# Kernel tuning notes

Measured on AMD Instinct MI355X. Metric: run time of the kernel, lower is better.

The kernel has to match this reference:

```python
import jax, jax.numpy as jnp
import numpy as np

N = 100000          # nodes
E = 1600000         # edges (before self-loops)
F_IN = 128          # raw node features
TOPO = 8            # topological feature dim
HEADS1, HID1 = 8, 8 # conv1: 8 heads x 8 channels, concat -> 64
C_OUT = 40          # classes (conv2: 1 head, no concat)
NEG_SLOPE = 0.2     # PyG GATConv leaky_relu slope


def setup_inputs() -> dict:
    key = jax.random.key(0)
    ks = jax.random.split(key, 12)
    x = jax.random.normal(ks[0], (N, F_IN), jnp.float32)
    topo = jax.random.normal(ks[1], (N, TOPO), jnp.float32)
    edge_index = jax.random.randint(ks[2], (2, E), 0, N, jnp.int32)
    s = 0.1
    W1 = jax.random.normal(ks[3], (F_IN + TOPO, HEADS1 * HID1), jnp.float32) * s
    a_src1 = jax.random.normal(ks[4], (HEADS1, HID1), jnp.float32) * s
    a_dst1 = jax.random.normal(ks[5], (HEADS1, HID1), jnp.float32) * s
    b1 = jnp.zeros((HEADS1 * HID1,), jnp.float32)
    W2 = jax.random.normal(ks[6], (HEADS1 * HID1, C_OUT), jnp.float32) * s
    a_src2 = jax.random.normal(ks[7], (1, C_OUT), jnp.float32) * s
    a_dst2 = jax.random.normal(ks[8], (1, C_OUT), jnp.float32) * s
    b2 = jnp.zeros((C_OUT,), jnp.float32)
    return {"x": x, "topo": topo, "edge_index": edge_index,
            "W1": W1, "a_src1": a_src1, "a_dst1": a_dst1, "b1": b1,
            "W2": W2, "a_src2": a_src2, "a_dst2": a_dst2, "b2": b2}


def _gat_conv(x, src, dst, W, a_src, a_dst, b, heads, concat):
    # x: [N, Fin]; src/dst: [Etot] (self-loops already included)
    n = x.shape[0]
    h = (x @ W).reshape(n, heads, -1)                 # [N, H, C]
    alpha_s = jnp.sum(h * a_src[None], axis=-1)       # [N, H]
    alpha_d = jnp.sum(h * a_dst[None], axis=-1)       # [N, H]
    e = jax.nn.leaky_relu(alpha_s[src] + alpha_d[dst], NEG_SLOPE)  # [Etot, H]
    # segment softmax over destination nodes (numerically stable)
    m = jax.ops.segment_max(e, dst, num_segments=n)   # [N, H]
    ex = jnp.exp(e - m[dst])
    z = jax.ops.segment_sum(ex, dst, num_segments=n)  # [N, H]
    alpha = ex / (z[dst] + 1e-16)                     # [Etot, H]
    out = jax.ops.segment_sum(h[src] * alpha[..., None], dst, num_segments=n)  # [N,H,C]
    out = out.reshape(n, -1) if concat else out.mean(axis=1)
    return out + b


def reference(x, topo, edge_index, W1, a_src1, a_dst1, b1, W2, a_src2, a_dst2, b2):
    n = x.shape[0]
    loops = jnp.arange(n, dtype=edge_index.dtype)
    src = jnp.concatenate([edge_index[0], loops])  # PyG add_self_loops=True
    dst = jnp.concatenate([edge_index[1], loops])
    h = jnp.concatenate([x, topo], axis=1)         # [N, F_IN + TOPO]
    # dropout is identity in eval mode
    h = jax.nn.elu(_gat_conv(h, src, dst, W1, a_src1, a_dst1, b1, HEADS1, True))
    logits = _gat_conv(h, src, dst, W2, a_src2, a_dst2, b2, 1, False)
    return jax.nn.log_softmax(logits, axis=1)
```

## Files before the change

### kernel.cpp

```cpp
#include <hip/hip_runtime.h>
#include <math.h>


#define NBUK_MAX 512
#define BIN_CHUNK 4096
#define BUK_CAP 4608

typedef unsigned short ushort_t;

__device__ inline unsigned int f2bf(float f) {
    unsigned int u = __float_as_uint(f);
    u += 0x7FFFu + ((u >> 16) & 1u);
    return u >> 16;
}
__device__ inline float bf_lo(unsigned int u) {
    return __uint_as_float(u << 16);
}
__device__ inline float bf_hi(unsigned int u) {
    return __uint_as_float(u & 0xFFFF0000u);
}
__device__ inline float lrelu_exp(float q) {
    return __expf(q >= 0.f ? q : 0.2f * q);
}

__device__ inline int wave_incl_scan(int v, int lane) {
    #pragma unroll
    for (int ofs = 1; ofs < 64; ofs <<= 1) {
        int t = __shfl_up(v, ofs);
        if (lane >= ofs) v += t;
    }
    return v;
}

__global__ __launch_bounds__(256) void k_bin(const int* __restrict__ src,
                                             const int* __restrict__ dst,
                                             int* __restrict__ gCursor,
                                             unsigned int* __restrict__ tmp,
                                             int E, int NBUK) {
    __shared__ int lcnt[NBUK_MAX];
    __shared__ int lcur[NBUK_MAX];
    int tid = threadIdx.x;
    int base = blockIdx.x * BIN_CHUNK;
    for (int i = tid; i < NBUK; i += 256) lcnt[i] = 0;
    __syncthreads();
    int d[16];
    #pragma unroll
    for (int q = 0; q < 4; q++) {
        int e = base + q * 1024 + 4 * tid;
        if (e + 3 < E) {
            int4 v = *(const int4*)&dst[e];
            d[4 * q + 0] = v.x; d[4 * q + 1] = v.y;
            d[4 * q + 2] = v.z; d[4 * q + 3] = v.w;
        } else {
            #pragma unroll
            for (int k = 0; k < 4; k++)
                d[4 * q + k] = (e + k < E) ? dst[e + k] : -1;
        }
    }
    #pragma unroll
    for (int k = 0; k < 16; k++)
        if (d[k] >= 0) atomicAdd(&lcnt[d[k] >> 8], 1);
    __syncthreads();
    for (int b = tid; b < NBUK; b += 256) {
        int c = lcnt[b];
        lcur[b] = c ? b * BUK_CAP + atomicAdd(&gCursor[b], c) : 0;
    }
    __syncthreads();
    #pragma unroll
    for (int q = 0; q < 4; q++) {
        int e = base + q * 1024 + 4 * tid;
        int s[4];
        if (e + 3 < E) {
            int4 v = *(const int4*)&src[e];
            s[0] = v.x; s[1] = v.y; s[2] = v.z; s[3] = v.w;
        } else {
            #pragma unroll
            for (int k = 0; k < 4; k++)
                s[k] = (e + k < E) ? src[e + k] : 0;
        }
        #pragma unroll
        for (int k = 0; k < 4; k++) {
            int dd = d[4 * q + k];
            if (dd >= 0) {
                int p = atomicAdd(&lcur[dd >> 8], 1);
                tmp[p] = ((unsigned int)s[k] << 8) | (unsigned int)(dd & 255);
            }
        }
    }
}

__global__ __launch_bounds__(512) void k_fill2(const unsigned int* __restrict__ tmp,
                                               const int* __restrict__ gCursor,
                                               int* __restrict__ rowptr,
                                               int* __restrict__ rowEnd,
                                               int* __restrict__ csr, int N) {
    __shared__ int cnt[256];
    __shared__ int cur[256];
    __shared__ int wsum[4];
    int b = blockIdx.x, tid = threadIdx.x;
    int e0 = b * BUK_CAP;
    int cnt_e = gCursor[b];
    int e1 = e0 + cnt_e;
    if (tid < 256) cnt[tid] = 0;
    __syncthreads();
    {
        int nq = cnt_e >> 2;
        const uint4* t4 = (const uint4*)(tmp + e0);
        for (int q = tid; q < nq; q += 512) {
            uint4 v = t4[q];
            atomicAdd(&cnt[v.x & 255u], 1);
            atomicAdd(&cnt[v.y & 255u], 1);
            atomicAdd(&cnt[v.z & 255u], 1);
            atomicAdd(&cnt[v.w & 255u], 1);
        }
        for (int i = (nq << 2) + tid; i < cnt_e; i += 512)
            atomicAdd(&cnt[tmp[e0 + i] & 255u], 1);
    }
    __syncthreads();
    if (tid < 256) {
        int lane = tid & 63, wv = tid >> 6;
        int v = cnt[tid];
        int incl = wave_incl_scan(v, lane);
        if (lane == 63) wsum[wv] = incl;
        cnt[tid] = incl - v;
    }
    __syncthreads();
    if (tid < 256) {
        int wv = tid >> 6;
        int woff = 0;
        for (int i = 0; i < wv; i++) woff += wsum[i];
        int excl = woff + cnt[tid];
        int node = b * 256 + tid;
        int start = e0 + excl;
        cur[tid] = start;
        if (node < N) {
            rowptr[node] = start;
        }
    }
    __syncthreads();
    if (tid < 256) {
        int node = b * 256 + tid;
        if (node < N) rowEnd[node] = (tid < 255) ? cur[tid + 1] : e1;
    }
    __syncthreads();
    for (int i = e0 + tid; i < e1; i += 512) {
        unsigned int t = tmp[i];
        int p = atomicAdd(&cur[t & 255u], 1);
        csr[p] = (int)(t >> 8);
    }
}

__global__ __launch_bounds__(256) void k_xform1(const float* __restrict__ x,
                                                const float* __restrict__ topo,
                                                const float* __restrict__ W1,
                                                const float* __restrict__ asrc,
                                                const float* __restrict__ adst,
                                                ushort_t* __restrict__ h1b,
                                                float* __restrict__ as1,
                                                float* __restrict__ ad1, int N) {
    __shared__ float XT[136 * 64];
    __shared__ float WS[136 * 64];
    int tid = threadIdx.x;
    int n0 = blockIdx.x * 64;
    {
        const float4* W4 = (const float4*)W1;
        float4* WS4 = (float4*)WS;
        for (int i = tid; i < 2176; i += 256) WS4[i] = W4[i];
    }
    {
        const float4* x4 = (const float4*)x;
        for (int i = tid; i < 2048; i += 256) {
            int node = i & 63, k4 = i >> 6;
            int gn = n0 + node; if (gn > N - 1) gn = N - 1;
            float4 v = x4[(size_t)gn * 32 + k4];
            int k = k4 * 4;
            XT[(k + 0) * 64 + node] = v.x;
            XT[(k + 1) * 64 + node] = v.y;
            XT[(k + 2) * 64 + node] = v.z;
            XT[(k + 3) * 64 + node] = v.w;
        }
        const float4* t4 = (const float4*)topo;
        if (tid < 128) {
            int node = tid & 63, j4 = tid >> 6;
            int gn = n0 + node; if (gn > N - 1) gn = N - 1;
            float4 v = t4[(size_t)gn * 2 + j4];
            int k = 128 + j4 * 4;
            XT[(k + 0) * 64 + node] = v.x;
            XT[(k + 1) * 64 + node] = v.y;
            XT[(k + 2) * 64 + node] = v.z;
            XT[(k + 3) * 64 + node] = v.w;
        }
    }
    __syncthreads();
    int ci = tid & 15, ni = tid >> 4;
    int nb = ni * 4, cb = ci * 4;
    float acc[16];
    #pragma unroll
    for (int i = 0; i < 16; i++) acc[i] = 0.f;
    #pragma unroll 4
    for (int k = 0; k < 136; k++) {
        float4 xv = *(const float4*)&XT[k * 64 + nb];
        float4 wv = *(const float4*)&WS[k * 64 + cb];
        acc[0]  = fmaf(xv.x, wv.x, acc[0]);  acc[1]  = fmaf(xv.x, wv.y, acc[1]);
        acc[2]  = fmaf(xv.x, wv.z, acc[2]);  acc[3]  = fmaf(xv.x, wv.w, acc[3]);
        acc[4]  = fmaf(xv.y, wv.x, acc[4]);  acc[5]  = fmaf(xv.y, wv.y, acc[5]);
        acc[6]  = fmaf(xv.y, wv.z, acc[6]);  acc[7]  = fmaf(xv.y, wv.w, acc[7]);
        acc[8]  = fmaf(xv.z, wv.x, acc[8]);  acc[9]  = fmaf(xv.z, wv.y, acc[9]);
        acc[10] = fmaf(xv.z, wv.z, acc[10]); acc[11] = fmaf(xv.z, wv.w, acc[11]);
        acc[12] = fmaf(xv.w, wv.x, acc[12]); acc[13] = fmaf(xv.w, wv.y, acc[13]);
        acc[14] = fmaf(xv.w, wv.z, acc[14]); acc[15] = fmaf(xv.w, wv.w, acc[15]);
    }
    int head = cb >> 3;
    #pragma unroll
    for (int i = 0; i < 4; i++) {
        int n = n0 + nb + i;
        unsigned int p0 = f2bf(acc[i * 4 + 0]) | (f2bf(acc[i * 4 + 1]) << 16);
        unsigned int p1 = f2bf(acc[i * 4 + 2]) | (f2bf(acc[i * 4 + 3]) << 16);
        if (n < N) *(uint2*)&h1b[(size_t)n * 64 + cb] = make_uint2(p0, p1);
        float s = 0.f, d = 0.f;
        #pragma unroll
        for (int j = 0; j < 4; j++) {
            s = fmaf(acc[i * 4 + j], asrc[cb + j], s);
            d = fmaf(acc[i * 4 + j], adst[cb + j], d);
        }
        s += __shfl_xor(s, 1);
        d += __shfl_xor(d, 1);
        if ((ci & 1) == 0 && n < N) {
            as1[n * 8 + head] = s;
            ad1[n * 8 + head] = d;
        }
    }
}

__global__ __launch_bounds__(256) void k_agg1(const ushort_t* __restrict__ h1b,
                                              const float* __restrict__ as1,
                                              const float* __restrict__ ad1,
                                              const float* __restrict__ b1,
                                              const int* __restrict__ rowptr,
                                              const int* __restrict__ rowEnd,
                                              const int* __restrict__ csr,
                                              float* __restrict__ h2, int N) {
    int tid = threadIdx.x, lane = tid & 63;
    int n = blockIdx.x * 4 + (tid >> 6);
    if (n >= N) return;
    int g = lane >> 5, p = lane & 31;
    int c0 = 2 * p;
    int h = p >> 2;
    const char* h1c = (const char*)h1b;
    const char* as1c = (const char*)as1;
    unsigned coff = (unsigned)(p << 2);
    unsigned whoff = (unsigned)((lane & 7) << 2);
    int wbase = (g << 3) + h;
    float ad_dl = ad1[n * 8 + h];
    float adv = ad1[n * 8 + (lane & 7)];
    float acc0 = 0.f, acc1 = 0.f, zl = 0.f;
    {
        float e0 = as1[n * 8 + h] + ad_dl;
        float w = lrelu_exp(e0);
        if (g == 0) {
            unsigned int u = *(const unsigned int*)(h1c + (((unsigned)n << 7) + coff));
            acc0 = w * bf_lo(u); acc1 = w * bf_hi(u); zl = w;
        }
    }
    int j0 = rowptr[n], j1 = rowEnd[n];
    int j = j0;
    for (; j + 8 <= j1; j += 8) {
        int cv = csr[j + (lane & 7)];
        int se = __shfl(cv, lane >> 3);
        float av = *(const float*)(as1c + (((unsigned)se << 5) + whoff));
        float wall = lrelu_exp(av + adv);
        int s0 = __shfl(cv, 0 + g);
        int s1 = __shfl(cv, 2 + g);
        int s2 = __shfl(cv, 4 + g);
        int s3 = __shfl(cv, 6 + g);
        unsigned int u0 = *(const unsigned int*)(h1c + (((unsigned)s0 << 7) + coff));
        unsigned int u1 = *(const unsigned int*)(h1c + (((unsigned)s1 << 7) + coff));
        unsigned int u2 = *(const unsigned int*)(h1c + (((unsigned)s2 << 7) + coff));
        unsigned int u3 = *(const unsigned int*)(h1c + (((unsigned)s3 << 7) + coff));
        float w0 = __shfl(wall, wbase);
        float w1 = __shfl(wall, wbase + 16);
        float w2 = __shfl(wall, wbase + 32);
        float w3 = __shfl(wall, wbase + 48);
        acc0 = fmaf(w0, bf_lo(u0), acc0); acc1 = fmaf(w0, bf_hi(u0), acc1); zl += w0;
        acc0 = fmaf(w1, bf_lo(u1), acc0); acc1 = fmaf(w1, bf_hi(u1), acc1); zl += w1;
        acc0 = fmaf(w2, bf_lo(u2), acc0); acc1 = fmaf(w2, bf_hi(u2), acc1); zl += w2;
        acc0 = fmaf(w3, bf_lo(u3), acc0); acc1 = fmaf(w3, bf_hi(u3), acc1); zl += w3;
    }
    int t = j1 - j;
    if (t > 0) {
        int idx = lane & 7; idx = idx < t ? idx : t - 1;
        int cv = csr[j + idx];
        int e_w = lane >> 3;
        int se = __shfl(cv, e_w);
        float av = *(const float*)(as1c + (((unsigned)se << 5) + whoff));
        float wall = (e_w < t) ? lrelu_exp(av + adv) : 0.f;
        #pragma unroll
        for (int i = 0; i < 4; i++) {
            int e = 2 * i + g;
            int s = __shfl(cv, e);
            unsigned int u = *(const unsigned int*)(h1c + (((unsigned)s << 7) + coff));
            float w = __shfl(wall, wbase + (i << 4));
            acc0 = fmaf(w, bf_lo(u), acc0); acc1 = fmaf(w, bf_hi(u), acc1); zl += w;
        }
    }
    float A0 = acc0 + __shfl_xor(acc0, 32);
    float A1 = acc1 + __shfl_xor(acc1, 32);
    float Z  = zl + __shfl_xor(zl, 32);
    if (g == 0) {
        float inv = 1.f / (Z + 1e-16f);
        float v0 = A0 * inv + b1[c0];
        float v1 = A1 * inv + b1[c0 + 1];
        v0 = v0 > 0.f ? v0 : (__expf(v0) - 1.f);
        v1 = v1 > 0.f ? v1 : (__expf(v1) - 1.f);
        *(float2*)&h2[(size_t)n * 64 + c0] = make_float2(v0, v1);
    }
}

__global__ __launch_bounds__(256) void k_xform2(const float* __restrict__ h2,
                                                const float* __restrict__ W2,
                                                const float* __restrict__ asrc2,
                                                const float* __restrict__ adst2,
                                                ushort_t* __restrict__ gb,
                                                float* __restrict__ as2,
                                                float* __restrict__ ad2, int N) {
    __shared__ float XT[64 * 64];
    __shared__ float WS[64 * 40];
    int tid = threadIdx.x;
    int n0 = blockIdx.x * 64;
    {
        const float4* W4 = (const float4*)W2;
        float4* WS4 = (float4*)WS;
        for (int i = tid; i < 640; i += 256) WS4[i] = W4[i];
    }
    {
        const float4* h4 = (const float4*)h2;
        for (int i = tid; i < 1024; i += 256) {
            int node = i & 63, k4 = i >> 6;
            int gn = n0 + node; if (gn > N - 1) gn = N - 1;
            float4 v = h4[(size_t)gn * 16 + k4];
            int k = k4 * 4;
            XT[(k + 0) * 64 + node] = v.x;
            XT[(k + 1) * 64 + node] = v.y;
            XT[(k + 2) * 64 + node] = v.z;
            XT[(k + 3) * 64 + node] = v.w;
        }
    }
    __syncthreads();
    int ci = tid & 15, ni = tid >> 4;
    int nb = ni * 4, cb = ci * 4;
    float acc[16];
    #pragma unroll
    for (int i = 0; i < 16; i++) acc[i] = 0.f;
    if (ci < 10) {
        #pragma unroll 4
        for (int k = 0; k < 64; k++) {
            float4 xv = *(const float4*)&XT[k * 64 + nb];
            float4 wv = *(const float4*)&WS[k * 40 + cb];
            acc[0]  = fmaf(xv.x, wv.x, acc[0]);  acc[1]  = fmaf(xv.x, wv.y, acc[1]);
            acc[2]  = fmaf(xv.x, wv.z, acc[2]);  acc[3]  = fmaf(xv.x, wv.w, acc[3]);
            acc[4]  = fmaf(xv.y, wv.x, acc[4]);  acc[5]  = fmaf(xv.y, wv.y, acc[5]);
            acc[6]  = fmaf(xv.y, wv.z, acc[6]);  acc[7]  = fmaf(xv.y, wv.w, acc[7]);
            acc[8]  = fmaf(xv.z, wv.x, acc[8]);  acc[9]  = fmaf(xv.z, wv.y, acc[9]);
            acc[10] = fmaf(xv.z, wv.z, acc[10]); acc[11] = fmaf(xv.z, wv.w, acc[11]);
            acc[12] = fmaf(xv.w, wv.x, acc[12]); acc[13] = fmaf(xv.w, wv.y, acc[13]);
            acc[14] = fmaf(xv.w, wv.z, acc[14]); acc[15] = fmaf(xv.w, wv.w, acc[15]);
        }
    }
    #pragma unroll
    for (int i = 0; i < 4; i++) {
        int n = n0 + nb + i;
        if (ci < 10 && n < N) {
            unsigned int p0 = f2bf(acc[i * 4 + 0]) | (f2bf(acc[i * 4 + 1]) << 16);
            unsigned int p1 = f2bf(acc[i * 4 + 2]) | (f2bf(acc[i * 4 + 3]) << 16);
            *(uint2*)&gb[(size_t)n * 40 + cb] = make_uint2(p0, p1);
        }
        float s = 0.f, d = 0.f;
        if (ci < 10) {
            #pragma unroll
            for (int j = 0; j < 4; j++) {
                s = fmaf(acc[i * 4 + j], asrc2[cb + j], s);
                d = fmaf(acc[i * 4 + j], adst2[cb + j], d);
            }
        }
        s += __shfl_xor(s, 1); s += __shfl_xor(s, 2);
        s += __shfl_xor(s, 4); s += __shfl_xor(s, 8);
        d += __shfl_xor(d, 1); d += __shfl_xor(d, 2);
        d += __shfl_xor(d, 4); d += __shfl_xor(d, 8);
        if (ci == 0 && n < N) { as2[n] = s; ad2[n] = d; }
    }
}

__global__ __launch_bounds__(256) void k_agg2(const ushort_t* __restrict__ gb,
                                              const float* __restrict__ as2,
                                              const float* __restrict__ ad2,
                                              const float* __restrict__ b2,
                                              const int* __restrict__ rowptr,
                                              const int* __restrict__ rowEnd,
                                              const int* __restrict__ csr,
                                              float* __restrict__ out, int N) {
    int tid = threadIdx.x, lane = tid & 63;
    int n = blockIdx.x * 4 + (tid >> 6);
    if (n >= N) return;
    int g = lane / 20, p = lane % 20;
    int c0 = 2 * p;
    const char* gbc = (const char*)gb;
    unsigned coff = (unsigned)(p << 2);
    int lm12 = lane % 12;
    float add = ad2[n];
    float acc0 = 0.f, acc1 = 0.f, zl = 0.f;
    {
        float e0 = as2[n] + add;
        float w = lrelu_exp(e0);
        if (g == 0) {
            unsigned int u = *(const unsigned int*)(gbc + ((unsigned)n * 80u + coff));
            acc0 = w * bf_lo(u); acc1 = w * bf_hi(u); zl = w;
        }
    }
    int j0 = rowptr[n], j1 = rowEnd[n];
    int j = j0;
    int gi0 = (0 + g) < 12 ? (0 + g) : 11;
    int gi1 = (3 + g) < 12 ? (3 + g) : 11;
    int gi2 = (6 + g) < 12 ? (6 + g) : 11;
    int gi3 = (9 + g) < 12 ? (9 + g) : 11;
    for (; j + 12 <= j1; j += 12) {
        int cv = csr[j + lm12];
        float av = as2[cv];
        float wall = lrelu_exp(av + add);
        int s0 = __shfl(cv, gi0);
        int s1 = __shfl(cv, gi1);
        int s2 = __shfl(cv, gi2);
        int s3 = __shfl(cv, gi3);
        unsigned int u0 = *(const unsigned int*)(gbc + ((unsigned)s0 * 80u + coff));
        unsigned int u1 = *(const unsigned int*)(gbc + ((unsigned)s1 * 80u + coff));
        unsigned int u2 = *(const unsigned int*)(gbc + ((unsigned)s2 * 80u + coff));
        unsigned int u3 = *(const unsigned int*)(gbc + ((unsigned)s3 * 80u + coff));
        float w0 = __shfl(wall, gi0);
        float w1 = __shfl(wall, gi1);
        float w2 = __shfl(wall, gi2);
        float w3 = __shfl(wall, gi3);
        acc0 = fmaf(w0, bf_lo(u0), acc0); acc1 = fmaf(w0, bf_hi(u0), acc1); zl += w0;
        acc0 = fmaf(w1, bf_lo(u1), acc0); acc1 = fmaf(w1, bf_hi(u1), acc1); zl += w1;
        acc0 = fmaf(w2, bf_lo(u2), acc0); acc1 = fmaf(w2, bf_hi(u2), acc1); zl += w2;
        acc0 = fmaf(w3, bf_lo(u3), acc0); acc1 = fmaf(w3, bf_hi(u3), acc1); zl += w3;
    }
    int t = j1 - j;
    if (t > 0) {
        int idx = lm12 < t ? lm12 : t - 1;
        int cv = csr[j + idx];
        float av = as2[cv];
        float wall = (lm12 < t) ? lrelu_exp(av + add) : 0.f;
        #pragma unroll
        for (int i = 0; i < 4; i++) {
            int e = 3 * i + g;
            int gi = e < 12 ? e : 11;
            int s = __shfl(cv, gi);
            unsigned int u = *(const unsigned int*)(gbc + ((unsigned)s * 80u + coff));
            float w = __shfl(wall, gi);
            acc0 = fmaf(w, bf_lo(u), acc0); acc1 = fmaf(w, bf_hi(u), acc1); zl += w;
        }
    }
    float A0 = acc0 + __shfl(acc0, (lane + 20) & 63) + __shfl(acc0, (lane + 40) & 63);
    float A1 = acc1 + __shfl(acc1, (lane + 20) & 63) + __shfl(acc1, (lane + 40) & 63);
    float Z  = zl + __shfl(zl, (lane + 20) & 63) + __shfl(zl, (lane + 40) & 63);
    float l0 = 0.f, l1 = 0.f;
    bool active = (lane < 20);
    if (active) {
        float inv = 1.f / (Z + 1e-16f);
        l0 = A0 * inv + b2[c0];
        l1 = A1 * inv + b2[c0 + 1];
    }
    float mv = active ? fmaxf(l0, l1) : -INFINITY;
    #pragma unroll
    for (int ofs = 1; ofs < 32; ofs <<= 1) mv = fmaxf(mv, __shfl_xor(mv, ofs));
    float ev = active ? (__expf(l0 - mv) + __expf(l1 - mv)) : 0.f;
    #pragma unroll
    for (int ofs = 1; ofs < 32; ofs <<= 1) ev += __shfl_xor(ev, ofs);
    if (active) {
        float ls = mv + __logf(ev);
        *(float2*)&out[(size_t)n * 40 + c0] = make_float2(l0 - ls, l1 - ls);
    }
}

extern "C" void kernel_launch(void* const* d_in, const int* in_sizes, int n_in,
                              void* d_out, int out_size, void* d_ws, size_t ws_size,
                              hipStream_t stream) {
    const float* x    = (const float*)d_in[0];
    const float* topo = (const float*)d_in[1];
    const int*   ei   = (const int*)d_in[2];
    const float* W1   = (const float*)d_in[3];
    const float* a_s1 = (const float*)d_in[4];
    const float* a_d1 = (const float*)d_in[5];
    const float* b1   = (const float*)d_in[6];
    const float* W2   = (const float*)d_in[7];
    const float* a_s2 = (const float*)d_in[8];
    const float* a_d2 = (const float*)d_in[9];
    const float* b2   = (const float*)d_in[10];
    float* out = (float*)d_out;

    int N = in_sizes[0] / 128;
    int E = in_sizes[2] / 2;
    const int* esrc = ei;
    const int* edst = ei + E;
    int NBUK = (N + 255) / 256;
    size_t cap = (size_t)NBUK * BUK_CAP;

    char* ws = (char*)d_ws;
    size_t off = 0;
    auto alloc = [&](size_t bytes) -> void* {
        void* p = ws + off;
        off = (off + bytes + 255) & ~(size_t)255;
        return p;
    };
    ushort_t* h1b  = (ushort_t*)alloc((size_t)N * 64 * 2);
    float* as1     = (float*)alloc((size_t)N * 8 * 4);
    float* ad1     = (float*)alloc((size_t)N * 8 * 4);
    float* h2      = (float*)alloc((size_t)N * 64 * 4);
    ushort_t* gb   = (ushort_t*)alloc((size_t)N * 40 * 2);
    float* as2     = (float*)alloc((size_t)N * 4);
    float* ad2     = (float*)alloc((size_t)N * 4);
    int*   rowptr  = (int*)alloc((size_t)N * 4);
    int*   rowEnd  = (int*)alloc((size_t)N * 4);
    int*   csr     = (int*)alloc(cap * 4);
    unsigned int* tmp = (unsigned int*)alloc(cap * 4);
    int* gCursor   = (int*)alloc((size_t)NBUK * 4);

    hipMemsetAsync(gCursor, 0, (size_t)NBUK * 4, stream);
    int nbin = (E + BIN_CHUNK - 1) / BIN_CHUNK;
    k_bin<<<nbin, 256, 0, stream>>>(esrc, edst, gCursor, tmp, E, NBUK);
    k_fill2<<<NBUK, 512, 0, stream>>>(tmp, gCursor, rowptr, rowEnd, csr, N);

    int nbg = (N + 63) / 64;
    int nb4 = (N + 3) / 4;
    k_xform1<<<nbg, 256, 0, stream>>>(x, topo, W1, a_s1, a_d1, h1b, as1, ad1, N);
    k_agg1<<<nb4, 256, 0, stream>>>(h1b, as1, ad1, b1, rowptr, rowEnd, csr, h2, N);
    k_xform2<<<nbg, 256, 0, stream>>>(h2, W2, a_s2, a_d2, gb, as2, ad2, N);
    k_agg2<<<nb4, 256, 0, stream>>>(gb, as2, ad2, b2, rowptr, rowEnd, csr, out, N);
}
```

Baseline: 311.3 us.

## Remap GAT aggregation lanes to 16-byte row loads and pad layer-2 rows

Measured after the change: 314.5 us. No clear change (+1.0%).

```diff
diff --git a/kernel.cpp b/kernel.cpp
--- a/kernel.cpp
+++ b/kernel.cpp
@@ -232,6 +232,19 @@
     }
 }
 
+#define AGG_FMA(W_, U_)                                           \
+    {                                                             \
+        acc[0] = fmaf(W_, bf_lo(U_.x), acc[0]);                   \
+        acc[1] = fmaf(W_, bf_hi(U_.x), acc[1]);                   \
+        acc[2] = fmaf(W_, bf_lo(U_.y), acc[2]);                   \
+        acc[3] = fmaf(W_, bf_hi(U_.y), acc[3]);                   \
+        acc[4] = fmaf(W_, bf_lo(U_.z), acc[4]);                   \
+        acc[5] = fmaf(W_, bf_hi(U_.z), acc[5]);                   \
+        acc[6] = fmaf(W_, bf_lo(U_.w), acc[6]);                   \
+        acc[7] = fmaf(W_, bf_hi(U_.w), acc[7]);                   \
+        z += W_;                                                  \
+    }
+
 __global__ __launch_bounds__(256) void k_agg1(const ushort_t* __restrict__ h1b,
                                               const float* __restrict__ as1,
                                               const float* __restrict__ ad1,
@@ -243,76 +256,77 @@
     int tid = threadIdx.x, lane = tid & 63;
     int n = blockIdx.x * 4 + (tid >> 6);
     if (n >= N) return;
-    int g = lane >> 5, p = lane & 31;
-    int c0 = 2 * p;
-    int h = p >> 2;
+    int g = lane >> 3;
+    int head = lane & 7;
     const char* h1c = (const char*)h1b;
-    const char* as1c = (const char*)as1;
-    unsigned coff = (unsigned)(p << 2);
-    unsigned whoff = (unsigned)((lane & 7) << 2);
-    int wbase = (g << 3) + h;
-    float ad_dl = ad1[n * 8 + h];
-    float adv = ad1[n * 8 + (lane & 7)];
-    float acc0 = 0.f, acc1 = 0.f, zl = 0.f;
-    {
-        float e0 = as1[n * 8 + h] + ad_dl;
-        float w = lrelu_exp(e0);
+    unsigned hoff = (unsigned)head << 4;
+    float adv = ad1[n * 8 + head];
+    float acc[8];
+    #pragma unroll
+    for (int k = 0; k < 8; k++) acc[k] = 0.f;
+    float z = 0.f;
+    {
+        float w = lrelu_exp(as1[n * 8 + head] + adv);
         if (g == 0) {
-            unsigned int u = *(const unsigned int*)(h1c + (((unsigned)n << 7) + coff));
-            acc0 = w * bf_lo(u); acc1 = w * bf_hi(u); zl = w;
-        }
-    }
-    int j0 = rowptr[n], j1 = rowEnd[n];
-    int j = j0;
-    for (; j + 8 <= j1; j += 8) {
+            uint4 u = *(const uint4*)(h1c + (((unsigned)n << 7) + hoff));
+            acc[0] = w * bf_lo(u.x); acc[1] = w * bf_hi(u.x);
+            acc[2] = w * bf_lo(u.y); acc[3] = w * bf_hi(u.y);
+            acc[4] = w * bf_lo(u.z); acc[5] = w * bf_hi(u.z);
+            acc[6] = w * bf_lo(u.w); acc[7] = w * bf_hi(u.w);
+            z = w;
+        }
+    }
+    int j = rowptr[n], j1 = rowEnd[n];
+    for (; j + 16 <= j1; j += 16) {
+        int cv = csr[j + (lane & 15)];
+        int se0 = __shfl(cv, g);
+        int se1 = __shfl(cv, 8 + g);
+        float av0 = as1[se0 * 8 + head];
+        float av1 = as1[se1 * 8 + head];
+        uint4 u0 = *(const uint4*)(h1c + (((unsigned)se0 << 7) + hoff));
+        uint4 u1 = *(const uint4*)(h1c + (((unsigned)se1 << 7) + hoff));
+        float w0 = lrelu_exp(av0 + adv);
+        float w1 = lrelu_exp(av1 + adv);
+        AGG_FMA(w0, u0);
+        AGG_FMA(w1, u1);
+    }
+    if (j + 8 <= j1) {
         int cv = csr[j + (lane & 7)];
-        int se = __shfl(cv, lane >> 3);
-        float av = *(const float*)(as1c + (((unsigned)se << 5) + whoff));
-        float wall = lrelu_exp(av + adv);
-        int s0 = __shfl(cv, 0 + g);
-        int s1 = __shfl(cv, 2 + g);
-        int s2 = __shfl(cv, 4 + g);
-        int s3 = __shfl(cv, 6 + g);
-        unsigned int u0 = *(const unsigned int*)(h1c + (((unsigned)s0 << 7) + coff));
-        unsigned int u1 = *(const unsigned int*)(h1c + (((unsigned)s1 << 7) + coff));
-        unsigned int u2 = *(const unsigned int*)(h1c + (((unsigned)s2 << 7) + coff));
-        unsigned int u3 = *(const unsigned int*)(h1c + (((unsigned)s3 << 7) + coff));
-        float w0 = __shfl(wall, wbase);
-        float w1 = __shfl(wall, wbase + 16);
-        float w2 = __shfl(wall, wbase + 32);
-        float w3 = __shfl(wall, wbase + 48);
-        acc0 = fmaf(w0, bf_lo(u0), acc0); acc1 = fmaf(w0, bf_hi(u0), acc1); zl += w0;
-        acc0 = fmaf(w1, bf_lo(u1), acc0); acc1 = fmaf(w1, bf_hi(u1), acc1); zl += w1;
-        acc0 = fmaf(w2, bf_lo(u2), acc0); acc1 = fmaf(w2, bf_hi(u2), acc1); zl += w2;
-        acc0 = fmaf(w3, bf_lo(u3), acc0); acc1 = fmaf(w3, bf_hi(u3), acc1); zl += w3;
+        int se = __shfl(cv, g);
+        float av = as1[se * 8 + head];
+        uint4 u = *(const uint4*)(h1c + (((unsigned)se << 7) + hoff));
+        float w = lrelu_exp(av + adv);
+        AGG_FMA(w, u);
+        j += 8;
     }
     int t = j1 - j;
     if (t > 0) {
-        int idx = lane & 7; idx = idx < t ? idx : t - 1;
+        int idx = (lane & 7); idx = idx < t ? idx : t - 1;
         int cv = csr[j + idx];
-        int e_w = lane >> 3;
-        int se = __shfl(cv, e_w);
-        float av = *(const float*)(as1c + (((unsigned)se << 5) + whoff));
-        float wall = (e_w < t) ? lrelu_exp(av + adv) : 0.f;
+        int ge = g < t ? g : t - 1;
+        int se = __shfl(cv, ge);
+        float w = (g < t) ? lrelu_exp(as1[se * 8 + head] + adv) : 0.f;
+        uint4 u = *(const uint4*)(h1c + (((unsigned)se << 7) + hoff));
+        AGG_FMA(w, u);
+    }
+    #pragma unroll
+    for (int k = 0; k < 8; k++) {
+        acc[k] += __shfl_xor(acc[k], 8);
+        acc[k] += __shfl_xor(acc[k], 16);
+        acc[k] += __shfl_xor(acc[k], 32);
+    }
+    z += __shfl_xor(z, 8); z += __shfl_xor(z, 16); z += __shfl_xor(z, 32);
+    if (g == 0) {
+        float inv = 1.f / (z + 1e-16f);
+        float o[8];
         #pragma unroll
-        for (int i = 0; i < 4; i++) {
-            int e = 2 * i + g;
-            int s = __shfl(cv, e);
-            unsigned int u = *(const unsigned int*)(h1c + (((unsigned)s << 7) + coff));
-            float w = __shfl(wall, wbase + (i << 4));
-            acc0 = fmaf(w, bf_lo(u), acc0); acc1 = fmaf(w, bf_hi(u), acc1); zl += w;
-        }
-    }
-    float A0 = acc0 + __shfl_xor(acc0, 32);
-    float A1 = acc1 + __shfl_xor(acc1, 32);
-    float Z  = zl + __shfl_xor(zl, 32);
-    if (g == 0) {
-        float inv = 1.f / (Z + 1e-16f);
-        float v0 = A0 * inv + b1[c0];
-        float v1 = A1 * inv + b1[c0 + 1];
-        v0 = v0 > 0.f ? v0 : (__expf(v0) - 1.f);
-        v1 = v1 > 0.f ? v1 : (__expf(v1) - 1.f);
-        *(float2*)&h2[(size_t)n * 64 + c0] = make_float2(v0, v1);
+        for (int k = 0; k < 8; k++) {
+            float v = acc[k] * inv + b1[head * 8 + k];
+            o[k] = v > 0.f ? v : (__expf(v) - 1.f);
+        }
+        float4* dp = (float4*)&h2[(size_t)n * 64 + head * 8];
+        dp[0] = make_float4(o[0], o[1], o[2], o[3]);
+        dp[1] = make_float4(o[4], o[5], o[6], o[7]);
     }
 }
 
@@ -372,7 +386,7 @@
         if (ci < 10 && n < N) {
             unsigned int p0 = f2bf(acc[i * 4 + 0]) | (f2bf(acc[i * 4 + 1]) << 16);
             unsigned int p1 = f2bf(acc[i * 4 + 2]) | (f2bf(acc[i * 4 + 3]) << 16);
-            *(uint2*)&gb[(size_t)n * 40 + cb] = make_uint2(p0, p1);
+            *(uint2*)&gb[(size_t)n * 64 + cb] = make_uint2(p0, p1);
         }
         float s = 0.f, d = 0.f;
         if (ci < 10) {
@@ -401,83 +415,95 @@
     int tid = threadIdx.x, lane = tid & 63;
     int n = blockIdx.x * 4 + (tid >> 6);
     if (n >= N) return;
-    int g = lane / 20, p = lane % 20;
-    int c0 = 2 * p;
+    int g = lane >> 3;
+    int p = lane & 7;
     const char* gbc = (const char*)gb;
-    unsigned coff = (unsigned)(p << 2);
-    int lm12 = lane % 12;
+    unsigned poff = (unsigned)p << 4;
     float add = ad2[n];
-    float acc0 = 0.f, acc1 = 0.f, zl = 0.f;
-    {
-        float e0 = as2[n] + add;
-        float w = lrelu_exp(e0);
+    float acc[8];
+    #pragma unroll
+    for (int k = 0; k < 8; k++) acc[k] = 0.f;
+    float z = 0.f;
+    {
+        float w = lrelu_exp(as2[n] + add);
         if (g == 0) {
-            unsigned int u = *(const unsigned int*)(gbc + ((unsigned)n * 80u + coff));
-            acc0 = w * bf_lo(u); acc1 = w * bf_hi(u); zl = w;
-        }
-    }
-    int j0 = rowptr[n], j1 = rowEnd[n];
-    int j = j0;
-    int gi0 = (0 + g) < 12 ? (0 + g) : 11;
-    int gi1 = (3 + g) < 12 ? (3 + g) : 11;
-    int gi2 = (6 + g) < 12 ? (6 + g) : 11;
-    int gi3 = (9 + g) < 12 ? (9 + g) : 11;
-    for (; j + 12 <= j1; j += 12) {
-        int cv = csr[j + lm12];
-        float av = as2[cv];
-        float wall = lrelu_exp(av + add);
-        int s0 = __shfl(cv, gi0);
-        int s1 = __shfl(cv, gi1);
-        int s2 = __shfl(cv, gi2);
-        int s3 = __shfl(cv, gi3);
-        unsigned int u0 = *(const unsigned int*)(gbc + ((unsigned)s0 * 80u + coff));
-        unsigned int u1 = *(const unsigned int*)(gbc + ((unsigned)s1 * 80u + coff));
-        unsigned int u2 = *(const unsigned int*)(gbc + ((unsigned)s2 * 80u + coff));
-        unsigned int u3 = *(const unsigned int*)(gbc + ((unsigned)s3 * 80u + coff));
-        float w0 = __shfl(wall, gi0);
-        float w1 = __shfl(wall, gi1);
-        float w2 = __shfl(wall, gi2);
-        float w3 = __shfl(wall, gi3);
-        acc0 = fmaf(w0, bf_lo(u0), acc0); acc1 = fmaf(w0, bf_hi(u0), acc1); zl += w0;
-        acc0 = fmaf(w1, bf_lo(u1), acc0); acc1 = fmaf(w1, bf_hi(u1), acc1); zl += w1;
-        acc0 = fmaf(w2, bf_lo(u2), acc0); acc1 = fmaf(w2, bf_hi(u2), acc1); zl += w2;
-        acc0 = fmaf(w3, bf_lo(u3), acc0); acc1 = fmaf(w3, bf_hi(u3), acc1); zl += w3;
+            uint4 u = *(const uint4*)(gbc + (((unsigned)n << 7) + poff));
+            acc[0] = w * bf_lo(u.x); acc[1] = w * bf_hi(u.x);
+            acc[2] = w * bf_lo(u.y); acc[3] = w * bf_hi(u.y);
+            acc[4] = w * bf_lo(u.z); acc[5] = w * bf_hi(u.z);
+            acc[6] = w * bf_lo(u.w); acc[7] = w * bf_hi(u.w);
+            z = w;
+        }
+    }
+    int j = rowptr[n], j1 = rowEnd[n];
+    for (; j + 16 <= j1; j += 16) {
+        int cv = csr[j + (lane & 15)];
+        int se0 = __shfl(cv, g);
+        int se1 = __shfl(cv, 8 + g);
+        float av0 = as2[se0];
+        float av1 = as2[se1];
+        uint4 u0 = *(const uint4*)(gbc + (((unsigned)se0 << 7) + poff));
+        uint4 u1 = *(const uint4*)(gbc + (((unsigned)se1 << 7) + poff));
+        float w0 = lrelu_exp(av0 + add);
+        float w1 = lrelu_exp(av1 + add);
+        AGG_FMA(w0, u0);
+        AGG_FMA(w1, u1);
+    }
+    if (j + 8 <= j1) {
+        int cv = csr[j + (lane & 7)];
+        int se = __shfl(cv, g);
+        float av = as2[se];
+        uint4 u = *(const uint4*)(gbc + (((unsigned)se << 7) + poff));
+        float w = lrelu_exp(av + add);
+        AGG_FMA(w, u);
+        j += 8;
     }
     int t = j1 - j;
     if (t > 0) {
-        int idx = lm12 < t ? lm12 : t - 1;
+        int idx = (lane & 7); idx = idx < t ? idx : t - 1;
         int cv = csr[j + idx];
-        float av = as2[cv];
-        float wall = (lm12 < t) ? lrelu_exp(av + add) : 0.f;
-        #pragma unroll
-        for (int i = 0; i < 4; i++) {
-            int e = 3 * i + g;
-            int gi = e < 12 ? e : 11;
-            int s = __shfl(cv, gi);
-            unsigned int u = *(const unsigned int*)(gbc + ((unsigned)s * 80u + coff));
-            float w = __shfl(wall, gi);
-            acc0 = fmaf(w, bf_lo(u), acc0); acc1 = fmaf(w, bf_hi(u), acc1); zl += w;
-        }
-    }
-    float A0 = acc0 + __shfl(acc0, (lane + 20) & 63) + __shfl(acc0, (lane + 40) & 63);
-    float A1 = acc1 + __shfl(acc1, (lane + 20) & 63) + __shfl(acc1, (lane + 40) & 63);
-    float Z  = zl + __shfl(zl, (lane + 20) & 63) + __shfl(zl, (lane + 40) & 63);
-    float l0 = 0.f, l1 = 0.f;
-    bool active = (lane < 20);
-    if (active) {
-        float inv = 1.f / (Z + 1e-16f);
-        l0 = A0 * inv + b2[c0];
-        l1 = A1 * inv + b2[c0 + 1];
-    }
-    float mv = active ? fmaxf(l0, l1) : -INFINITY;
-    #pragma unroll
-    for (int ofs = 1; ofs < 32; ofs <<= 1) mv = fmaxf(mv, __shfl_xor(mv, ofs));
-    float ev = active ? (__expf(l0 - mv) + __expf(l1 - mv)) : 0.f;
-    #pragma unroll
-    for (int ofs = 1; ofs < 32; ofs <<= 1) ev += __shfl_xor(ev, ofs);
-    if (active) {
-        float ls = mv + __logf(ev);
-        *(float2*)&out[(size_t)n * 40 + c0] = make_float2(l0 - ls, l1 - ls);
+        int ge = g < t ? g : t - 1;
+        int se = __shfl(cv, ge);
+        float w = (g < t) ? lrelu_exp(as2[se] + add) : 0.f;
+        uint4 u = *(const uint4*)(gbc + (((unsigned)se << 7) + poff));
+        AGG_FMA(w, u);
+    }
+    #pragma unroll
+    for (int k = 0; k < 8; k++) {
+        acc[k] += __shfl_xor(acc[k], 8);
+        acc[k] += __shfl_xor(acc[k], 16);
+        acc[k] += __shfl_xor(acc[k], 32);
+    }
+    z += __shfl_xor(z, 8); z += __shfl_xor(z, 16); z += __shfl_xor(z, 32);
+    if (g == 0) {
+        bool act = (p < 5);
+        float inv = 1.f / (z + 1e-16f);
+        float l[8];
+        float mv = -INFINITY;
+        if (act) {
+            #pragma unroll
+            for (int k = 0; k < 8; k++) {
+                l[k] = acc[k] * inv + b2[p * 8 + k];
+                mv = fmaxf(mv, l[k]);
+            }
+        }
+        mv = fmaxf(mv, __shfl_xor(mv, 1));
+        mv = fmaxf(mv, __shfl_xor(mv, 2));
+        mv = fmaxf(mv, __shfl_xor(mv, 4));
+        float ev = 0.f;
+        if (act) {
+            #pragma unroll
+            for (int k = 0; k < 8; k++) ev += __expf(l[k] - mv);
+        }
+        ev += __shfl_xor(ev, 1);
+        ev += __shfl_xor(ev, 2);
+        ev += __shfl_xor(ev, 4);
+        if (act) {
+            float ls = mv + __logf(ev);
+            float4* dp = (float4*)&out[(size_t)n * 40 + p * 8];
+            dp[0] = make_float4(l[0] - ls, l[1] - ls, l[2] - ls, l[3] - ls);
+            dp[1] = make_float4(l[4] - ls, l[5] - ls, l[6] - ls, l[7] - ls);
+        }
     }
 }
 
@@ -515,7 +541,7 @@
     float* as1     = (float*)alloc((size_t)N * 8 * 4);
     float* ad1     = (float*)alloc((size_t)N * 8 * 4);
     float* h2      = (float*)alloc((size_t)N * 64 * 4);
-    ushort_t* gb   = (ushort_t*)alloc((size_t)N * 40 * 2);
+    ushort_t* gb   = (ushort_t*)alloc((size_t)N * 64 * 2);
     float* as2     = (float*)alloc((size_t)N * 4);
     float* ad2     = (float*)alloc((size_t)N * 4);
     int*   rowptr  = (int*)alloc((size_t)N * 4);
```

## Remap agg1 lanes to head-per-lane with 16-byte row loads

Applied to the files above, without the earlier changes.

New measurement: 308.8 us. No clear change (-0.8%).

```diff
diff --git a/kernel.cpp b/kernel.cpp
--- a/kernel.cpp
+++ b/kernel.cpp
@@ -232,6 +232,19 @@
     }
 }
 
+#define AGG_FMA(W_, U_)                                           \
+    {                                                             \
+        acc[0] = fmaf(W_, bf_lo(U_.x), acc[0]);                   \
+        acc[1] = fmaf(W_, bf_hi(U_.x), acc[1]);                   \
+        acc[2] = fmaf(W_, bf_lo(U_.y), acc[2]);                   \
+        acc[3] = fmaf(W_, bf_hi(U_.y), acc[3]);                   \
+        acc[4] = fmaf(W_, bf_lo(U_.z), acc[4]);                   \
+        acc[5] = fmaf(W_, bf_hi(U_.z), acc[5]);                   \
+        acc[6] = fmaf(W_, bf_lo(U_.w), acc[6]);                   \
+        acc[7] = fmaf(W_, bf_hi(U_.w), acc[7]);                   \
+        z += W_;                                                  \
+    }
+
 __global__ __launch_bounds__(256) void k_agg1(const ushort_t* __restrict__ h1b,
                                               const float* __restrict__ as1,
                                               const float* __restrict__ ad1,
@@ -243,76 +256,77 @@
     int tid = threadIdx.x, lane = tid & 63;
     int n = blockIdx.x * 4 + (tid >> 6);
     if (n >= N) return;
-    int g = lane >> 5, p = lane & 31;
-    int c0 = 2 * p;
-    int h = p >> 2;
+    int g = lane >> 3;
+    int head = lane & 7;
     const char* h1c = (const char*)h1b;
-    const char* as1c = (const char*)as1;
-    unsigned coff = (unsigned)(p << 2);
-    unsigned whoff = (unsigned)((lane & 7) << 2);
-    int wbase = (g << 3) + h;
-    float ad_dl = ad1[n * 8 + h];
-    float adv = ad1[n * 8 + (lane & 7)];
-    float acc0 = 0.f, acc1 = 0.f, zl = 0.f;
-    {
-        float e0 = as1[n * 8 + h] + ad_dl;
-        float w = lrelu_exp(e0);
+    unsigned hoff = (unsigned)head << 4;
+    float adv = ad1[n * 8 + head];
+    float acc[8];
+    #pragma unroll
+    for (int k = 0; k < 8; k++) acc[k] = 0.f;
+    float z = 0.f;
+    {
+        float w = lrelu_exp(as1[n * 8 + head] + adv);
         if (g == 0) {
-            unsigned int u = *(const unsigned int*)(h1c + (((unsigned)n << 7) + coff));
-            acc0 = w * bf_lo(u); acc1 = w * bf_hi(u); zl = w;
-        }
-    }
-    int j0 = rowptr[n], j1 = rowEnd[n];
-    int j = j0;
-    for (; j + 8 <= j1; j += 8) {
+            uint4 u = *(const uint4*)(h1c + (((unsigned)n << 7) + hoff));
+            acc[0] = w * bf_lo(u.x); acc[1] = w * bf_hi(u.x);
+            acc[2] = w * bf_lo(u.y); acc[3] = w * bf_hi(u.y);
+            acc[4] = w * bf_lo(u.z); acc[5] = w * bf_hi(u.z);
+            acc[6] = w * bf_lo(u.w); acc[7] = w * bf_hi(u.w);
+            z = w;
+        }
+    }
+    int j = rowptr[n], j1 = rowEnd[n];
+    for (; j + 16 <= j1; j += 16) {
+        int cv = csr[j + (lane & 15)];
+        int se0 = __shfl(cv, g);
+        int se1 = __shfl(cv, 8 + g);
+        float av0 = as1[se0 * 8 + head];
+        float av1 = as1[se1 * 8 + head];
+        uint4 u0 = *(const uint4*)(h1c + (((unsigned)se0 << 7) + hoff));
+        uint4 u1 = *(const uint4*)(h1c + (((unsigned)se1 << 7) + hoff));
+        float w0 = lrelu_exp(av0 + adv);
+        float w1 = lrelu_exp(av1 + adv);
+        AGG_FMA(w0, u0);
+        AGG_FMA(w1, u1);
+    }
+    if (j + 8 <= j1) {
         int cv = csr[j + (lane & 7)];
-        int se = __shfl(cv, lane >> 3);
-        float av = *(const float*)(as1c + (((unsigned)se << 5) + whoff));
-        float wall = lrelu_exp(av + adv);
-        int s0 = __shfl(cv, 0 + g);
-        int s1 = __shfl(cv, 2 + g);
-        int s2 = __shfl(cv, 4 + g);
-        int s3 = __shfl(cv, 6 + g);
-        unsigned int u0 = *(const unsigned int*)(h1c + (((unsigned)s0 << 7) + coff));
-        unsigned int u1 = *(const unsigned int*)(h1c + (((unsigned)s1 << 7) + coff));
-        unsigned int u2 = *(const unsigned int*)(h1c + (((unsigned)s2 << 7) + coff));
-        unsigned int u3 = *(const unsigned int*)(h1c + (((unsigned)s3 << 7) + coff));
-        float w0 = __shfl(wall, wbase);
-        float w1 = __shfl(wall, wbase + 16);
-        float w2 = __shfl(wall, wbase + 32);
-        float w3 = __shfl(wall, wbase + 48);
-        acc0 = fmaf(w0, bf_lo(u0), acc0); acc1 = fmaf(w0, bf_hi(u0), acc1); zl += w0;
-        acc0 = fmaf(w1, bf_lo(u1), acc0); acc1 = fmaf(w1, bf_hi(u1), acc1); zl += w1;
-        acc0 = fmaf(w2, bf_lo(u2), acc0); acc1 = fmaf(w2, bf_hi(u2), acc1); zl += w2;
-        acc0 = fmaf(w3, bf_lo(u3), acc0); acc1 = fmaf(w3, bf_hi(u3), acc1); zl += w3;
+        int se = __shfl(cv, g);
+        float av = as1[se * 8 + head];
+        uint4 u = *(const uint4*)(h1c + (((unsigned)se << 7) + hoff));
+        float w = lrelu_exp(av + adv);
+        AGG_FMA(w, u);
+        j += 8;
     }
     int t = j1 - j;
     if (t > 0) {
-        int idx = lane & 7; idx = idx < t ? idx : t - 1;
+        int idx = (lane & 7); idx = idx < t ? idx : t - 1;
         int cv = csr[j + idx];
-        int e_w = lane >> 3;
-        int se = __shfl(cv, e_w);
-        float av = *(const float*)(as1c + (((unsigned)se << 5) + whoff));
-        float wall = (e_w < t) ? lrelu_exp(av + adv) : 0.f;
+        int ge = g < t ? g : t - 1;
+        int se = __shfl(cv, ge);
+        float w = (g < t) ? lrelu_exp(as1[se * 8 + head] + adv) : 0.f;
+        uint4 u = *(const uint4*)(h1c + (((unsigned)se << 7) + hoff));
+        AGG_FMA(w, u);
+    }
+    #pragma unroll
+    for (int k = 0; k < 8; k++) {
+        acc[k] += __shfl_xor(acc[k], 8);
+        acc[k] += __shfl_xor(acc[k], 16);
+        acc[k] += __shfl_xor(acc[k], 32);
+    }
+    z += __shfl_xor(z, 8); z += __shfl_xor(z, 16); z += __shfl_xor(z, 32);
+    if (g == 0) {
+        float inv = 1.f / (z + 1e-16f);
+        float o[8];
         #pragma unroll
-        for (int i = 0; i < 4; i++) {
-            int e = 2 * i + g;
-            int s = __shfl(cv, e);
-            unsigned int u = *(const unsigned int*)(h1c + (((unsigned)s << 7) + coff));
-            float w = __shfl(wall, wbase + (i << 4));
-            acc0 = fmaf(w, bf_lo(u), acc0); acc1 = fmaf(w, bf_hi(u), acc1); zl += w;
-        }
-    }
-    float A0 = acc0 + __shfl_xor(acc0, 32);
-    float A1 = acc1 + __shfl_xor(acc1, 32);
-    float Z  = zl + __shfl_xor(zl, 32);
-    if (g == 0) {
-        float inv = 1.f / (Z + 1e-16f);
-        float v0 = A0 * inv + b1[c0];
-        float v1 = A1 * inv + b1[c0 + 1];
-        v0 = v0 > 0.f ? v0 : (__expf(v0) - 1.f);
-        v1 = v1 > 0.f ? v1 : (__expf(v1) - 1.f);
-        *(float2*)&h2[(size_t)n * 64 + c0] = make_float2(v0, v1);
+        for (int k = 0; k < 8; k++) {
+            float v = acc[k] * inv + b1[head * 8 + k];
+            o[k] = v > 0.f ? v : (__expf(v) - 1.f);
+        }
+        float4* dp = (float4*)&h2[(size_t)n * 64 + head * 8];
+        dp[0] = make_float4(o[0], o[1], o[2], o[3]);
+        dp[1] = make_float4(o[4], o[5], o[6], o[7]);
     }
 }
 
```
